# Performance work log

Hardware: AMD Instinct MI355X
Metric: run time of the kernel (lower is better)

The kernel has to match this reference:

```python
import jax, jax.numpy as jnp
import numpy as np

N_HEADS = 16

def _rel_emb(table, len_q, len_k):
    # table: [2P+1, d] -> [len_q, len_k, d] via clipped relative distance lookup
    P = (table.shape[0] - 1) // 2
    rel = jnp.arange(len_k)[None, :] - jnp.arange(len_q)[:, None]
    idx = jnp.clip(rel, -P, P) + P
    return table[idx]

def setup_inputs() -> dict:
    key = jax.random.key(0)
    ks = jax.random.split(key, 13)
    B, S, E = 2, 2048, 1024
    P = 128
    d = E // N_HEADS
    s = 0.02
    return {
        "q": jax.random.normal(ks[0], (B, S, E), jnp.float32),
        "k": jax.random.normal(ks[1], (B, S, E), jnp.float32),
        "v": jax.random.normal(ks[2], (B, S, E), jnp.float32),
        "Wq": jax.random.normal(ks[3], (E, E), jnp.float32) * s,
        "bq": jnp.zeros((E,), jnp.float32),
        "Wk": jax.random.normal(ks[4], (E, E), jnp.float32) * s,
        "bk": jnp.zeros((E,), jnp.float32),
        "Wv": jax.random.normal(ks[5], (E, E), jnp.float32) * s,
        "bv": jnp.zeros((E,), jnp.float32),
        "Wo": jax.random.normal(ks[6], (E, E), jnp.float32) * s,
        "bo": jnp.zeros((E,), jnp.float32),
        "rk_table": jax.random.normal(ks[7], (2 * P + 1, d), jnp.float32) * s,
        "rv_table": jax.random.normal(ks[8], (2 * P + 1, d), jnp.float32) * s,
    }

def reference(q, k, v, Wq, bq, Wk, bk, Wv, bv, Wo, bo, rk_table, rv_table):
    B, Sq, E = q.shape
    Sk = k.shape[1]
    H = N_HEADS
    d = E // H
    scale = jnp.sqrt(jnp.asarray(d, q.dtype))

    qh = (q @ Wq.T + bq).reshape(B, Sq, H, d).transpose(0, 2, 1, 3)  # [B,H,Sq,d]
    kh = (k @ Wk.T + bk).reshape(B, Sk, H, d).transpose(0, 2, 1, 3)
    vh = (v @ Wv.T + bv).reshape(B, Sk, H, d).transpose(0, 2, 1, 3)

    qk = jnp.einsum('bhqd,bhkd->bhqk', qh, kh)
    r_k = _rel_emb(rk_table, Sq, Sk)                 # [Sq,Sk,d]
    q_rk = jnp.einsum('bhqd,qkd->bhqk', qh, r_k)
    attn = jax.nn.softmax((qk + q_rk) / scale, axis=-1)  # dropout p=0

    w1 = jnp.einsum('bhqk,bhkd->bhqd', attn, vh)
    r_v = _rel_emb(rv_table, Sq, Sk)
    w2 = jnp.einsum('bhqk,qkd->bhqd', attn, r_v)

    out = (w1 + w2).transpose(0, 2, 1, 3).reshape(B, Sq, E)
    return out @ Wo.T + bo
```

## Files before the change

### kernel.cpp

```cpp
#include <hip/hip_runtime.h>
#include <hip/hip_bf16.h>
#include <cstdint>
#include <cstddef>

#define NH   16
#define DH   64
#define SQ   2048
#define NB   2
#define EM   1024
#define NREL 257
#define QSTR 258
#define SCL  0.18033688f

typedef unsigned short ushort_t;
using bf16x8 = __attribute__((ext_vector_type(8))) __bf16;
using bf16x4 = __attribute__((ext_vector_type(4))) __bf16;
using f32x4  = __attribute__((ext_vector_type(4))) float;
#define MFMA16(a, b, c) __builtin_amdgcn_mfma_f32_16x16x32_bf16(a, b, c, 0, 0, 0)

__device__ __forceinline__ ushort_t f2bf(float f) {
    union { __bf16 h; ushort_t u; } x; x.h = (__bf16)f; return x.u;
}
__device__ __forceinline__ float bf2f(ushort_t u) {
    union { unsigned u; float f; } x; x.u = ((unsigned)u) << 16;
    return x.f;
}
__device__ __forceinline__ uint2 pack4(float a, float b, float c, float d) {
    union { bf16x4 v; uint2 u; } x;
    x.v = (bf16x4){ (__bf16)a, (__bf16)b, (__bf16)c, (__bf16)d };
    return x.u;
}
__device__ __forceinline__ int kperm(int x) {
    return (x & ~63) | ((x & 15) << 2) | ((x >> 4) & 3);
}

__global__ __launch_bounds__(256)
void cvt3(const float* __restrict__ a, const float* __restrict__ b,
          const float* __restrict__ c, ushort_t* __restrict__ oa,
          ushort_t* __restrict__ ob, ushort_t* __restrict__ oc, int n)
{
    const float* in = blockIdx.y == 0 ? a : (blockIdx.y == 1 ? b : c);
    ushort_t* out   = blockIdx.y == 0 ? oa : (blockIdx.y == 1 ? ob : oc);
    int i = (blockIdx.x * 256 + threadIdx.x) * 8;
    if (i < n) {
        float4 v0 = *reinterpret_cast<const float4*>(in + i);
        float4 v1 = *reinterpret_cast<const float4*>(in + i + 4);
        uint2 lo = pack4(v0.x, v0.y, v0.z, v0.w);
        uint2 hi = pack4(v1.x, v1.y, v1.z, v1.w);
        *reinterpret_cast<uint4*>(out + i) = make_uint4(lo.x, lo.y, hi.x, hi.y);
    }
}
__global__ __launch_bounds__(256)
void cvt4(const float* __restrict__ a, const float* __restrict__ b,
          const float* __restrict__ c, const float* __restrict__ d,
          ushort_t* __restrict__ oa, ushort_t* __restrict__ ob,
          ushort_t* __restrict__ oc, ushort_t* __restrict__ od, int n)
{
    const float* in = blockIdx.y == 0 ? a : (blockIdx.y == 1 ? b :
                      (blockIdx.y == 2 ? c : d));
    ushort_t* out   = blockIdx.y == 0 ? oa : (blockIdx.y == 1 ? ob :
                      (blockIdx.y == 2 ? oc : od));
    int i = (blockIdx.x * 256 + threadIdx.x) * 8;
    if (i < n) {
        float4 v0 = *reinterpret_cast<const float4*>(in + i);
        float4 v1 = *reinterpret_cast<const float4*>(in + i + 4);
        uint2 lo = pack4(v0.x, v0.y, v0.z, v0.w);
        uint2 hi = pack4(v1.x, v1.y, v1.z, v1.w);
        *reinterpret_cast<uint4*>(out + i) = make_uint4(lo.x, lo.y, hi.x, hi.y);
    }
}

__global__ __launch_bounds__(256)
void prep_tables(const float* __restrict__ rv, const float* __restrict__ rk,
                 ushort_t* __restrict__ rvT, ushort_t* __restrict__ rkb)
{
    int idx = blockIdx.x * 256 + threadIdx.x;
    if (idx < 64 * 256) {
        int d = idx >> 8, c = idx & 255;
        rvT[d * 256 + kperm(c)] = f2bf(rv[(size_t)(c + 1) * DH + d]);
    }
    idx -= 64 * 256;
    if (idx >= 0 && idx < 272 * 64) {
        int j = idx >> 6, d2 = idx & 63;
        rkb[idx] = (j < NREL) ? f2bf(rk[(size_t)j * DH + d2]) : (ushort_t)0;
    }
}

template<int MODE>
__global__ __launch_bounds__(256)
void gemm_bt(const ushort_t* __restrict__ A, const ushort_t* __restrict__ W,
             const float* __restrict__ bias, void* __restrict__ dstv,
             int M, int N, int K)
{
    __shared__ ushort_t As[128 * 40];
    __shared__ ushort_t Bs[128 * 40];
    const int t = threadIdx.x, lane = t & 63;
    const int wv = t >> 6, wr = wv >> 1, wc = wv & 1;
    const int g = lane >> 4, c16 = lane & 15;

    const int nwg = gridDim.x * gridDim.y;
    int flat = blockIdx.y * gridDim.x + blockIdx.x;
    int rm = (flat & 7) * (nwg >> 3) + (flat >> 3);
    const int n0 = (rm % gridDim.x) * 128;
    const int m0 = (rm / gridDim.x) * 128;

    f32x4 acc[4][4];
#pragma unroll
    for (int i = 0; i < 4; ++i)
#pragma unroll
        for (int j = 0; j < 4; ++j) acc[i][j] = (f32x4){0.f, 0.f, 0.f, 0.f};

    for (int k0 = 0; k0 < K; k0 += 32) {
        __syncthreads();
#pragma unroll
        for (int l = 0; l < 2; ++l) {
            const int fid = t + 256 * l;
            const int row = fid >> 2, ch = fid & 3;
            uint4 av = *reinterpret_cast<const uint4*>(A + (size_t)(m0 + row) * K + k0 + ch * 8);
            uint4 wv4 = *reinterpret_cast<const uint4*>(W + (size_t)(n0 + row) * K + k0 + ch * 8);
            *reinterpret_cast<uint4*>(As + row * 40 + ch * 8) = av;
            *reinterpret_cast<uint4*>(Bs + row * 40 + ch * 8) = wv4;
        }
        __syncthreads();

        bf16x8 af[4], bfr[4];
#pragma unroll
        for (int i = 0; i < 4; ++i)
            af[i] = *reinterpret_cast<const bf16x8*>(As + (wr * 64 + i * 16 + c16) * 40 + g * 8);
#pragma unroll
        for (int j = 0; j < 4; ++j)
            bfr[j] = *reinterpret_cast<const bf16x8*>(Bs + (wc * 64 + j * 16 + c16) * 40 + g * 8);
#pragma unroll
        for (int i = 0; i < 4; ++i)
#pragma unroll
            for (int j = 0; j < 4; ++j)
                acc[i][j] = MFMA16(af[i], bfr[j], acc[i][j]);
    }

#pragma unroll
    for (int j = 0; j < 4; ++j) {
        const int n = n0 + wc * 64 + j * 16 + c16;
        const float bn = bias[n];
#pragma unroll
        for (int i = 0; i < 4; ++i) {
#pragma unroll
            for (int r = 0; r < 4; ++r) {
                const int m = m0 + wr * 64 + i * 16 + 4 * g + r;
                const float vv = acc[i][j][r] + bn;
                if (MODE == 0) {
                    ((float*)dstv)[(size_t)m * N + n] = vv;
                } else {
                    const int b = m >> 11, s = m & (SQ - 1);
                    const int h = n >> 6, dd = n & 63;
                    if (MODE == 1) {
                        ((ushort_t*)dstv)[(((size_t)b * NH + h) * SQ + s) * DH + dd] = f2bf(vv);
                    } else {
                        const int sp = kperm(s);
                        ((ushort_t*)dstv)[(((size_t)b * NH + h) * DH + dd) * SQ + sp] = f2bf(vv);
                    }
                }
            }
        }
    }
}

__global__ __launch_bounds__(256)
void qrel_mfma(const ushort_t* __restrict__ qh, const ushort_t* __restrict__ rkb,
               ushort_t* __restrict__ qrel)
{
    const int t = threadIdx.x, lane = t & 63, w = t >> 6;
    const int g = lane >> 4, c16 = lane & 15;
    const size_t r0 = (size_t)blockIdx.x * 64 + w * 16;

    bf16x8 af[2];
#pragma unroll
    for (int ks = 0; ks < 2; ++ks)
        af[ks] = *reinterpret_cast<const bf16x8*>(qh + (r0 + c16) * DH + ks * 32 + g * 8);

    f32x4 acc[17];
#pragma unroll
    for (int n = 0; n < 17; ++n) acc[n] = (f32x4){0.f, 0.f, 0.f, 0.f};
#pragma unroll
    for (int n = 0; n < 17; ++n)
#pragma unroll
        for (int ks = 0; ks < 2; ++ks) {
            bf16x8 bf = *reinterpret_cast<const bf16x8*>(
                rkb + (size_t)(16 * n + c16) * DH + ks * 32 + g * 8);
            acc[n] = MFMA16(af[ks], bf, acc[n]);
        }
#pragma unroll
    for (int n = 0; n < 17; ++n) {
        const int j = 16 * n + c16;
        if (j < NREL) {
#pragma unroll
            for (int r = 0; r < 4; ++r)
                qrel[(r0 + 4 * g + r) * QSTR + j] = f2bf(acc[n][r] * SCL);
        }
    }
}

__global__ __launch_bounds__(256, 4)
void attn_flash(const ushort_t* __restrict__ qh, const ushort_t* __restrict__ kh,
                const ushort_t* __restrict__ vt, const ushort_t* __restrict__ qrel,
                ushort_t* __restrict__ Ptile, float* __restrict__ w1g,
                float* __restrict__ lacg, float* __restrict__ b0g,
                float* __restrict__ b256g)
{
    __shared__ ushort_t Ks[64 * 72];
    __shared__ ushort_t Vs[64 * 72];
    __shared__ ushort_t PQs[64 * 72];

    const int t = threadIdx.x, lane = t & 63, w = t >> 6;
    const int g = lane >> 4, c16 = lane & 15;
    const int nwg = gridDim.x * gridDim.y;
    int flat = blockIdx.y * gridDim.x + blockIdx.x;
    int rmid = (flat & 7) * (nwg >> 3) + (flat >> 3);
    const int q0 = (rmid & 31) * 64;
    const int bh = rmid >> 5;
    const size_t Gbase = ((size_t)bh * 32 + (q0 >> 6)) * 5;

#pragma unroll
    for (int l = 0; l < 2; ++l) {
        const int fid = t + 256 * l;
        const int row = fid >> 3, ch = fid & 7;
        uint4 v = *reinterpret_cast<const uint4*>(
            qh + ((size_t)bh * SQ + q0 + row) * DH + ch * 8);
        *reinterpret_cast<uint4*>(PQs + row * 72 + ch * 8) = v;
    }
    __syncthreads();
    bf16x8 qf[2];
#pragma unroll
    for (int ks = 0; ks < 2; ++ks)
        qf[ks] = *reinterpret_cast<const bf16x8*>(PQs + (w * 16 + c16) * 72 + ks * 32 + g * 8);

    float q0add[4], q256add[4];
#pragma unroll
    for (int i = 0; i < 4; ++i) {
        const size_t r = (size_t)bh * SQ + q0 + w * 16 + 4 * g + i;
        q0add[i]   = bf2f(qrel[r * QSTR + 0]);
        q256add[i] = bf2f(qrel[r * QSTR + 256]);
    }

    f32x4 w1[4];
#pragma unroll
    for (int n = 0; n < 4; ++n) w1[n] = (f32x4){0.f, 0.f, 0.f, 0.f};
    float lac[4] = {0.f,0.f,0.f,0.f}, b0[4] = {0.f,0.f,0.f,0.f}, b256[4] = {0.f,0.f,0.f,0.f};

    const int row_l = t >> 3, ch_l = t & 7;
    const int row_h = row_l + 32;
    uint4 kr0, kr1, vr0, vr1;
    {
        kr0 = *reinterpret_cast<const uint4*>(kh + ((size_t)bh * SQ + row_l) * DH + ch_l * 8);
        kr1 = *reinterpret_cast<const uint4*>(kh + ((size_t)bh * SQ + row_h) * DH + ch_l * 8);
        vr0 = *reinterpret_cast<const uint4*>(vt + ((size_t)bh * DH + row_l) * SQ + ch_l * 8);
        vr1 = *reinterpret_cast<const uint4*>(vt + ((size_t)bh * DH + row_h) * SQ + ch_l * 8);
    }

    for (int k0 = 0; k0 < SQ; k0 += 64) {
        __syncthreads();
        *reinterpret_cast<uint4*>(Ks + row_l * 72 + ch_l * 8) = kr0;
        *reinterpret_cast<uint4*>(Ks + row_h * 72 + ch_l * 8) = kr1;
        *reinterpret_cast<uint4*>(Vs + row_l * 72 + ch_l * 8) = vr0;
        *reinterpret_cast<uint4*>(Vs + row_h * 72 + ch_l * 8) = vr1;
        __syncthreads();
        if (k0 + 64 < SQ) {
            kr0 = *reinterpret_cast<const uint4*>(kh + ((size_t)bh * SQ + k0 + 64 + row_l) * DH + ch_l * 8);
            kr1 = *reinterpret_cast<const uint4*>(kh + ((size_t)bh * SQ + k0 + 64 + row_h) * DH + ch_l * 8);
            vr0 = *reinterpret_cast<const uint4*>(vt + ((size_t)bh * DH + row_l) * SQ + k0 + 64 + ch_l * 8);
            vr1 = *reinterpret_cast<const uint4*>(vt + ((size_t)bh * DH + row_h) * SQ + k0 + 64 + ch_l * 8);
        }

        f32x4 s[4];
#pragma unroll
        for (int n = 0; n < 4; ++n) s[n] = (f32x4){0.f, 0.f, 0.f, 0.f};
        __builtin_amdgcn_s_setprio(1);
#pragma unroll
        for (int ks = 0; ks < 2; ++ks)
#pragma unroll
            for (int n = 0; n < 4; ++n) {
                bf16x8 kf = *reinterpret_cast<const bf16x8*>(
                    Ks + (16 * n + c16) * 72 + ks * 32 + g * 8);
                s[n] = MFMA16(qf[ks], kf, s[n]);
            }
        __builtin_amdgcn_s_setprio(0);

        const int rel0 = k0 - q0;
        float rsum[4] = {0.f, 0.f, 0.f, 0.f};
        if (rel0 <= -192 || rel0 >= 192) {
            const bool lo = rel0 < 0;
#pragma unroll
            for (int i = 0; i < 4; ++i) {
                const float add = lo ? q0add[i] : q256add[i];
#pragma unroll
                for (int n = 0; n < 4; ++n) {
                    const float p = exp2f(fmaf(s[n][i], SCL, add));
                    s[n][i] = p; rsum[i] += p;
                }
                if (lo) b0[i] += rsum[i]; else b256[i] += rsum[i];
                *reinterpret_cast<uint2*>(PQs + (w * 16 + 4 * g + i) * 72 + c16 * 4) =
                    pack4(s[0][i], s[1][i], s[2][i], s[3][i]);
            }
        } else if (rel0 == -128 || rel0 == 128) {
            const int tix = (rel0 >> 6) + 2;
#pragma unroll
            for (int i = 0; i < 4; ++i) {
                const int qloc = w * 16 + 4 * g + i;
                const int qg = q0 + qloc;
                const ushort_t* qrow = qrel + ((size_t)bh * SQ + qg) * QSTR;
                float z[4];
#pragma unroll
                for (int n = 0; n < 4; ++n) {
                    const int rel = (k0 + 16 * n + c16) - qg;
                    const int idx = rel < -128 ? 0 : (rel > 128 ? 256 : rel + 128);
                    const float p = exp2f(fmaf(s[n][i], SCL, bf2f(qrow[idx])));
                    s[n][i] = p; rsum[i] += p;
                    const bool inb = (rel >= -127) & (rel <= 127);
                    z[n] = inb ? p : 0.f;
                    if (rel <= -128)      b0[i] += p;
                    else if (rel >= 128)  b256[i] += p;
                }
                *reinterpret_cast<uint2*>(PQs + qloc * 72 + c16 * 4) =
                    pack4(s[0][i], s[1][i], s[2][i], s[3][i]);
                *reinterpret_cast<uint2*>(
                    Ptile + ((Gbase + tix) * 64 + qloc) * 64 + 4 * c16) =
                    pack4(z[0], z[1], z[2], z[3]);
            }
        } else {
            const int tix = (rel0 >> 6) + 2;
#pragma unroll
            for (int i = 0; i < 4; ++i) {
                const int qloc = w * 16 + 4 * g + i;
                const int qg = q0 + qloc;
                const ushort_t* qrow = qrel + ((size_t)bh * SQ + qg) * QSTR;
#pragma unroll
                for (int n = 0; n < 4; ++n) {
                    const int rel = (k0 + 16 * n + c16) - qg;
                    const float p = exp2f(fmaf(s[n][i], SCL, bf2f(qrow[rel + 128])));
                    s[n][i] = p; rsum[i] += p;
                }
                const uint2 pk = pack4(s[0][i], s[1][i], s[2][i], s[3][i]);
                *reinterpret_cast<uint2*>(PQs + qloc * 72 + c16 * 4) = pk;
                *reinterpret_cast<uint2*>(
                    Ptile + ((Gbase + tix) * 64 + qloc) * 64 + 4 * c16) = pk;
            }
        }
#pragma unroll
        for (int i = 0; i < 4; ++i) lac[i] += rsum[i];

        __builtin_amdgcn_s_setprio(1);
#pragma unroll
        for (int ks = 0; ks < 2; ++ks) {
            bf16x8 pf = *reinterpret_cast<const bf16x8*>(
                PQs + (w * 16 + c16) * 72 + ks * 32 + g * 8);
#pragma unroll
            for (int n = 0; n < 4; ++n) {
                bf16x8 vf = *reinterpret_cast<const bf16x8*>(
                    Vs + (16 * n + c16) * 72 + ks * 32 + g * 8);
                w1[n] = MFMA16(pf, vf, w1[n]);
            }
        }
        __builtin_amdgcn_s_setprio(0);
    }

#pragma unroll
    for (int m = 1; m < 16; m <<= 1)
#pragma unroll
        for (int i = 0; i < 4; ++i) {
            lac[i]  += __shfl_xor(lac[i],  m, 64);
            b0[i]   += __shfl_xor(b0[i],   m, 64);
            b256[i] += __shfl_xor(b256[i], m, 64);
        }
    if (c16 == 0) {
#pragma unroll
        for (int i = 0; i < 4; ++i) {
            const size_t row = (size_t)bh * SQ + q0 + w * 16 + 4 * g + i;
            lacg[row] = lac[i]; b0g[row] = b0[i]; b256g[row] = b256[i];
        }
    }
#pragma unroll
    for (int n = 0; n < 4; ++n)
#pragma unroll
        for (int i = 0; i < 4; ++i) {
            const size_t row = (size_t)bh * SQ + q0 + w * 16 + 4 * g + i;
            w1g[row * DH + 16 * n + c16] = w1[n][i];
        }
}

__global__ __launch_bounds__(256)
void band_gemm(const ushort_t* __restrict__ Ptile, const ushort_t* __restrict__ rvT,
               const float* __restrict__ rv_f32, const float* __restrict__ w1g,
               const float* __restrict__ lacg, const float* __restrict__ b0g,
               const float* __restrict__ b256g, ushort_t* __restrict__ wout)
{
    __shared__ ushort_t Pband[64 * 264];
    const int t = threadIdx.x, lane = t & 63, w = t >> 6;
    const int g = lane >> 4, c16 = lane & 15;
    const int G = blockIdx.x;
    const size_t r0 = (size_t)G * 64;
    const int q0 = (G & 31) * 64;

    for (int i = t; i < 64 * 264 / 2; i += 256)
        reinterpret_cast<unsigned*>(Pband)[i] = 0u;
    __syncthreads();

    for (int u = t; u < 5 * 64 * 16; u += 256) {
        const int tix = u >> 10;
        const int kt0 = q0 + (tix - 2) * 64;
        if (kt0 < 0 || kt0 >= SQ) continue;
        const int qloc = (u >> 4) & 63;
        const int c = u & 15;
        uint2 pv = *reinterpret_cast<const uint2*>(
            Ptile + (((size_t)G * 5 + tix) * 64 + qloc) * 64 + 4 * c);
        const ushort_t* pe = reinterpret_cast<const ushort_t*>(&pv);
        const int relbase = (tix - 2) * 64 - qloc + 127;
#pragma unroll
        for (int n = 0; n < 4; ++n) {
            const int x = relbase + 16 * n + c;
            if (x >= 0 && x <= 254)
                Pband[qloc * 264 + ((x & ~63) | ((x & 15) << 2) | ((x >> 4) & 3))] = pe[n];
        }
    }
    if (t < 64) Pband[t * 264 + 255] = f2bf(b256g[r0 + t]);
    __syncthreads();

    f32x4 acc[4];
#pragma unroll
    for (int n = 0; n < 4; ++n) acc[n] = (f32x4){0.f, 0.f, 0.f, 0.f};
#pragma unroll
    for (int ks = 0; ks < 8; ++ks) {
        bf16x8 pm = *reinterpret_cast<const bf16x8*>(
            Pband + (w * 16 + c16) * 264 + ks * 32 + g * 8);
#pragma unroll
        for (int n = 0; n < 4; ++n) {
            bf16x8 rf = *reinterpret_cast<const bf16x8*>(
                rvT + (size_t)(16 * n + c16) * 256 + ks * 32 + g * 8);
            acc[n] = MFMA16(pm, rf, acc[n]);
        }
    }

#pragma unroll
    for (int i = 0; i < 4; ++i) {
        const size_t row = r0 + w * 16 + 4 * g + i;
        const float inv = 1.0f / lacg[row];
        const float vb0 = b0g[row];
        const int b = (int)(row >> 15), h = (int)((row >> 11) & 15), s = (int)(row & 2047);
#pragma unroll
        for (int n = 0; n < 4; ++n) {
            const int col = 16 * n + c16;
            const float val = (w1g[row * DH + col] + acc[n][i] + vb0 * rv_f32[col]) * inv;
            wout[(((size_t)b * SQ + s) * NH + h) * DH + col] = f2bf(val);
        }
    }
}

extern "C" void kernel_launch(void* const* d_in, const int* in_sizes, int n_in,
                              void* d_out, int out_size, void* d_ws, size_t ws_size,
                              hipStream_t stream)
{
    const float* q  = (const float*)d_in[0];
    const float* k  = (const float*)d_in[1];
    const float* v  = (const float*)d_in[2];
    const float* Wq = (const float*)d_in[3];
    const float* bq = (const float*)d_in[4];
    const float* Wk = (const float*)d_in[5];
    const float* bk = (const float*)d_in[6];
    const float* Wv = (const float*)d_in[7];
    const float* bv = (const float*)d_in[8];
    const float* Wo = (const float*)d_in[9];
    const float* bo = (const float*)d_in[10];
    const float* rk = (const float*)d_in[11];
    const float* rv = (const float*)d_in[12];

    char* ws = (char*)d_ws;
    auto alloc = [&](size_t bytes) { char* p = ws; ws += bytes; return p; };
    const size_t QB = (size_t)NB * SQ * EM * 2;
    const size_t WB = (size_t)EM * EM * 2;
    const size_t NR = (size_t)NB * NH * SQ;

    char* region0 = alloc(NR * 320 * 2);
    ushort_t* Ptile = (ushort_t*)region0;
    ushort_t* qbf = (ushort_t*)region0;
    ushort_t* kbf = (ushort_t*)(region0 + QB);
    ushort_t* vbf = (ushort_t*)(region0 + 2 * QB);
    ushort_t* Wqb = (ushort_t*)(region0 + 3 * QB);
    ushort_t* Wkb = (ushort_t*)(region0 + 3 * QB + WB);
    ushort_t* Wvb = (ushort_t*)(region0 + 3 * QB + 2 * WB);

    ushort_t* Wob  = (ushort_t*)alloc(WB);
    ushort_t* qhb  = (ushort_t*)alloc(QB);
    ushort_t* khb  = (ushort_t*)alloc(QB);
    ushort_t* vtb  = (ushort_t*)alloc(QB);
    ushort_t* wbuf = (ushort_t*)alloc(QB);
    ushort_t* rvT  = (ushort_t*)alloc(64 * 256 * 2);
    ushort_t* rkb  = (ushort_t*)alloc(272 * 64 * 2);
    ushort_t* qrel = (ushort_t*)alloc(NR * QSTR * 2);
    float*    w1g  = (float*)alloc(NR * DH * 4);
    float*    lacg = (float*)alloc(NR * 4);
    float*    b0g  = (float*)alloc(NR * 4);
    float*    b256g= (float*)alloc(NR * 4);

    const int NQ = NB * SQ * EM;
    const int NW = EM * EM;
    cvt3<<<dim3(NQ / 2048, 3), 256, 0, stream>>>(q, k, v, qbf, kbf, vbf, NQ);
    cvt4<<<dim3(NW / 2048, 4), 256, 0, stream>>>(Wq, Wk, Wv, Wo, Wqb, Wkb, Wvb, Wob, NW);
    prep_tables<<<132, 256, 0, stream>>>(rv, rk, rvT, rkb);

    const int M = NB * SQ;
    dim3 gg(EM / 128, M / 128);
    gemm_bt<1><<<gg, 256, 0, stream>>>(qbf, Wqb, bq, qhb, M, EM, EM);
    gemm_bt<1><<<gg, 256, 0, stream>>>(kbf, Wkb, bk, khb, M, EM, EM);
    gemm_bt<2><<<gg, 256, 0, stream>>>(vbf, Wvb, bv, vtb, M, EM, EM);
    qrel_mfma<<<(int)(NR / 64), 256, 0, stream>>>(qhb, rkb, qrel);

    attn_flash<<<dim3(32, 32), 256, 0, stream>>>(qhb, khb, vtb, qrel,
                                                 Ptile, w1g, lacg, b0g, b256g);
    band_gemm<<<(int)(NR / 64), 256, 0, stream>>>(Ptile, rvT, rv, w1g, lacg,
                                                  b0g, b256g, wbuf);
    gemm_bt<0><<<gg, 256, 0, stream>>>(wbuf, Wob, bo, d_out, M, EM, EM);
}
```

Measured before the change: 279.8 us.

## Fuse fp32-to-bf16 conversion into GEMM loads and enlarge attention query tile

Removes the standalone conversion kernels for activations and weights, converting fp32 to bf16 inside the GEMM tile loads instead. The flash-attention kernel now processes 128 queries per block (two 64-row subtiles per wave) to reuse K/V tiles from LDS, uses XOR-swizzled LDS layouts in place of padded rows, and drops to 2 blocks per CU. The band tiles, band_gemm indexing and workspace layout are adjusted to match, with wbuf aliased onto qrel. In exchange, the GEMMs now read fp32 weights and activations from global memory every tile, and occupancy for attention is lower.

```diff
diff --git a/kernel.cpp b/kernel.cpp
--- a/kernel.cpp
+++ b/kernel.cpp
@@ -33,41 +33,8 @@
 __device__ __forceinline__ int kperm(int x) {
     return (x & ~63) | ((x & 15) << 2) | ((x >> 4) & 3);
 }
-
-__global__ __launch_bounds__(256)
-void cvt3(const float* __restrict__ a, const float* __restrict__ b,
-          const float* __restrict__ c, ushort_t* __restrict__ oa,
-          ushort_t* __restrict__ ob, ushort_t* __restrict__ oc, int n)
-{
-    const float* in = blockIdx.y == 0 ? a : (blockIdx.y == 1 ? b : c);
-    ushort_t* out   = blockIdx.y == 0 ? oa : (blockIdx.y == 1 ? ob : oc);
-    int i = (blockIdx.x * 256 + threadIdx.x) * 8;
-    if (i < n) {
-        float4 v0 = *reinterpret_cast<const float4*>(in + i);
-        float4 v1 = *reinterpret_cast<const float4*>(in + i + 4);
-        uint2 lo = pack4(v0.x, v0.y, v0.z, v0.w);
-        uint2 hi = pack4(v1.x, v1.y, v1.z, v1.w);
-        *reinterpret_cast<uint4*>(out + i) = make_uint4(lo.x, lo.y, hi.x, hi.y);
-    }
-}
-__global__ __launch_bounds__(256)
-void cvt4(const float* __restrict__ a, const float* __restrict__ b,
-          const float* __restrict__ c, const float* __restrict__ d,
-          ushort_t* __restrict__ oa, ushort_t* __restrict__ ob,
-          ushort_t* __restrict__ oc, ushort_t* __restrict__ od, int n)
-{
-    const float* in = blockIdx.y == 0 ? a : (blockIdx.y == 1 ? b :
-                      (blockIdx.y == 2 ? c : d));
-    ushort_t* out   = blockIdx.y == 0 ? oa : (blockIdx.y == 1 ? ob :
-                      (blockIdx.y == 2 ? oc : od));
-    int i = (blockIdx.x * 256 + threadIdx.x) * 8;
-    if (i < n) {
-        float4 v0 = *reinterpret_cast<const float4*>(in + i);
-        float4 v1 = *reinterpret_cast<const float4*>(in + i + 4);
-        uint2 lo = pack4(v0.x, v0.y, v0.z, v0.w);
-        uint2 hi = pack4(v1.x, v1.y, v1.z, v1.w);
-        *reinterpret_cast<uint4*>(out + i) = make_uint4(lo.x, lo.y, hi.x, hi.y);
-    }
+__device__ __forceinline__ int lswz(int row, int byteoff) {
+    return row * 128 + (byteoff ^ ((row & 7) << 4));
 }
 
 __global__ __launch_bounds__(256)
@@ -86,9 +53,9 @@
     }
 }
 
-template<int MODE>
+template<int MODE, int ACVT>
 __global__ __launch_bounds__(256)
-void gemm_bt(const ushort_t* __restrict__ A, const ushort_t* __restrict__ W,
+void gemm_bt(const void* __restrict__ Av, const float* __restrict__ Wf,
              const float* __restrict__ bias, void* __restrict__ dstv,
              int M, int N, int K)
 {
@@ -116,10 +83,23 @@
         for (int l = 0; l < 2; ++l) {
             const int fid = t + 256 * l;
             const int row = fid >> 2, ch = fid & 3;
-            uint4 av = *reinterpret_cast<const uint4*>(A + (size_t)(m0 + row) * K + k0 + ch * 8);
-            uint4 wv4 = *reinterpret_cast<const uint4*>(W + (size_t)(n0 + row) * K + k0 + ch * 8);
-            *reinterpret_cast<uint4*>(As + row * 40 + ch * 8) = av;
-            *reinterpret_cast<uint4*>(Bs + row * 40 + ch * 8) = wv4;
+            if (ACVT) {
+                const float* Af = (const float*)Av;
+                float4 a0 = *reinterpret_cast<const float4*>(Af + (size_t)(m0 + row) * K + k0 + ch * 8);
+                float4 a1 = *reinterpret_cast<const float4*>(Af + (size_t)(m0 + row) * K + k0 + ch * 8 + 4);
+                uint2 lo = pack4(a0.x, a0.y, a0.z, a0.w);
+                uint2 hi = pack4(a1.x, a1.y, a1.z, a1.w);
+                *reinterpret_cast<uint4*>(As + row * 40 + ch * 8) = make_uint4(lo.x, lo.y, hi.x, hi.y);
+            } else {
+                const ushort_t* Ab = (const ushort_t*)Av;
+                *reinterpret_cast<uint4*>(As + row * 40 + ch * 8) =
+                    *reinterpret_cast<const uint4*>(Ab + (size_t)(m0 + row) * K + k0 + ch * 8);
+            }
+            float4 w0 = *reinterpret_cast<const float4*>(Wf + (size_t)(n0 + row) * K + k0 + ch * 8);
+            float4 w1_ = *reinterpret_cast<const float4*>(Wf + (size_t)(n0 + row) * K + k0 + ch * 8 + 4);
+            uint2 lo = pack4(w0.x, w0.y, w0.z, w0.w);
+            uint2 hi = pack4(w1_.x, w1_.y, w1_.z, w1_.w);
+            *reinterpret_cast<uint4*>(Bs + row * 40 + ch * 8) = make_uint4(lo.x, lo.y, hi.x, hi.y);
         }
         __syncthreads();
 
@@ -199,69 +179,74 @@
     }
 }
 
-__global__ __launch_bounds__(256, 4)
+__global__ __launch_bounds__(256, 2)
 void attn_flash(const ushort_t* __restrict__ qh, const ushort_t* __restrict__ kh,
                 const ushort_t* __restrict__ vt, const ushort_t* __restrict__ qrel,
                 ushort_t* __restrict__ Ptile, float* __restrict__ w1g,
                 float* __restrict__ lacg, float* __restrict__ b0g,
                 float* __restrict__ b256g)
 {
-    __shared__ ushort_t Ks[64 * 72];
-    __shared__ ushort_t Vs[64 * 72];
-    __shared__ ushort_t PQs[64 * 72];
+    __shared__ ushort_t Ks[64 * 64];
+    __shared__ ushort_t Vs[64 * 64];
+    __shared__ ushort_t PQs[128 * 64];
+    char* Ksb = (char*)Ks; char* Vsb = (char*)Vs; char* PQb = (char*)PQs;
 
     const int t = threadIdx.x, lane = t & 63, w = t >> 6;
     const int g = lane >> 4, c16 = lane & 15;
-    const int nwg = gridDim.x * gridDim.y;
     int flat = blockIdx.y * gridDim.x + blockIdx.x;
-    int rmid = (flat & 7) * (nwg >> 3) + (flat >> 3);
-    const int q0 = (rmid & 31) * 64;
-    const int bh = rmid >> 5;
-    const size_t Gbase = ((size_t)bh * 32 + (q0 >> 6)) * 5;
-
-#pragma unroll
-    for (int l = 0; l < 2; ++l) {
+    int rmid = (flat & 7) * 64 + (flat >> 3);
+    const int q0 = (rmid & 15) * 128;
+    const int bh = rmid >> 4;
+    const size_t Gbase = (size_t)rmid * 6;
+
+#pragma unroll
+    for (int l = 0; l < 4; ++l) {
         const int fid = t + 256 * l;
         const int row = fid >> 3, ch = fid & 7;
         uint4 v = *reinterpret_cast<const uint4*>(
             qh + ((size_t)bh * SQ + q0 + row) * DH + ch * 8);
-        *reinterpret_cast<uint4*>(PQs + row * 72 + ch * 8) = v;
+        *reinterpret_cast<uint4*>(PQb + lswz(row, ch * 16)) = v;
     }
     __syncthreads();
-    bf16x8 qf[2];
-#pragma unroll
-    for (int ks = 0; ks < 2; ++ks)
-        qf[ks] = *reinterpret_cast<const bf16x8*>(PQs + (w * 16 + c16) * 72 + ks * 32 + g * 8);
-
-    float q0add[4], q256add[4];
-#pragma unroll
-    for (int i = 0; i < 4; ++i) {
-        const size_t r = (size_t)bh * SQ + q0 + w * 16 + 4 * g + i;
-        q0add[i]   = bf2f(qrel[r * QSTR + 0]);
-        q256add[i] = bf2f(qrel[r * QSTR + 256]);
-    }
-
-    f32x4 w1[4];
-#pragma unroll
-    for (int n = 0; n < 4; ++n) w1[n] = (f32x4){0.f, 0.f, 0.f, 0.f};
-    float lac[4] = {0.f,0.f,0.f,0.f}, b0[4] = {0.f,0.f,0.f,0.f}, b256[4] = {0.f,0.f,0.f,0.f};
+    bf16x8 qf[2][2];
+#pragma unroll
+    for (int st = 0; st < 2; ++st)
+#pragma unroll
+        for (int ks = 0; ks < 2; ++ks)
+            qf[st][ks] = *reinterpret_cast<const bf16x8*>(
+                PQb + lswz(w * 16 + st * 64 + c16, ks * 64 + g * 16));
+
+    float q0add[2][4], q256add[2][4];
+#pragma unroll
+    for (int st = 0; st < 2; ++st)
+#pragma unroll
+        for (int i = 0; i < 4; ++i) {
+            const size_t r = (size_t)bh * SQ + q0 + w * 16 + st * 64 + 4 * g + i;
+            q0add[st][i]   = bf2f(qrel[r * QSTR + 0]);
+            q256add[st][i] = bf2f(qrel[r * QSTR + 256]);
+        }
+
+    f32x4 w1[2][4];
+#pragma unroll
+    for (int st = 0; st < 2; ++st)
+#pragma unroll
+        for (int n = 0; n < 4; ++n) w1[st][n] = (f32x4){0.f, 0.f, 0.f, 0.f};
+    float lac[2][4] = {}, b0[2][4] = {}, b256[2][4] = {};
 
     const int row_l = t >> 3, ch_l = t & 7;
     const int row_h = row_l + 32;
     uint4 kr0, kr1, vr0, vr1;
-    {
-        kr0 = *reinterpret_cast<const uint4*>(kh + ((size_t)bh * SQ + row_l) * DH + ch_l * 8);
-        kr1 = *reinterpret_cast<const uint4*>(kh + ((size_t)bh * SQ + row_h) * DH + ch_l * 8);
-        vr0 = *reinterpret_cast<const uint4*>(vt + ((size_t)bh * DH + row_l) * SQ + ch_l * 8);
-        vr1 = *reinterpret_cast<const uint4*>(vt + ((size_t)bh * DH + row_h) * SQ + ch_l * 8);
-    }
+    kr0 = *reinterpret_cast<const uint4*>(kh + ((size_t)bh * SQ + row_l) * DH + ch_l * 8);
+    kr1 = *reinterpret_cast<const uint4*>(kh + ((size_t)bh * SQ + row_h) * DH + ch_l * 8);
+    vr0 = *reinterpret_cast<const uint4*>(vt + ((size_t)bh * DH + row_l) * SQ + ch_l * 8);
+    vr1 = *reinterpret_cast<const uint4*>(vt + ((size_t)bh * DH + row_h) * SQ + ch_l * 8);
 
     for (int k0 = 0; k0 < SQ; k0 += 64) {
         __syncthreads();
-        *reinterpret_cast<uint4*>(Ks + row_l * 72 + ch_l * 8) = kr0;
-        *reinterpret_cast<uint4*>(Ks + row_h * 72 + ch_l * 8) = kr1;
-        *reinterpret_cast<uint4*>(Vs + row_l * 72 + ch_l * 8) = vr0;
-        *reinterpret_cast<uint4*>(Vs + row_h * 72 + ch_l * 8) = vr1;
+        *reinterpret_cast<uint4*>(Ksb + lswz(row_l, ch_l * 16)) = kr0;
+        *reinterpret_cast<uint4*>(Ksb + lswz(row_h, ch_l * 16)) = kr1;
+        *reinterpret_cast<uint4*>(Vsb + lswz(row_l, ch_l * 16)) = vr0;
+        *reinterpret_cast<uint4*>(Vsb + lswz(row_h, ch_l * 16)) = vr1;
         __syncthreads();
         if (k0 + 64 < SQ) {
             kr0 = *reinterpret_cast<const uint4*>(kh + ((size_t)bh * SQ + k0 + 64 + row_l) * DH + ch_l * 8);
@@ -270,120 +255,141 @@
             vr1 = *reinterpret_cast<const uint4*>(vt + ((size_t)bh * DH + row_h) * SQ + k0 + 64 + ch_l * 8);
         }
 
-        f32x4 s[4];
-#pragma unroll
-        for (int n = 0; n < 4; ++n) s[n] = (f32x4){0.f, 0.f, 0.f, 0.f};
-        __builtin_amdgcn_s_setprio(1);
-#pragma unroll
-        for (int ks = 0; ks < 2; ++ks)
-#pragma unroll
-            for (int n = 0; n < 4; ++n) {
-                bf16x8 kf = *reinterpret_cast<const bf16x8*>(
-                    Ks + (16 * n + c16) * 72 + ks * 32 + g * 8);
-                s[n] = MFMA16(qf[ks], kf, s[n]);
+        f32x4 s[2][4];
+#pragma unroll
+        for (int st = 0; st < 2; ++st)
+#pragma unroll
+            for (int n = 0; n < 4; ++n) s[st][n] = (f32x4){0.f, 0.f, 0.f, 0.f};
+        {
+            bf16x8 kf[4][2];
+#pragma unroll
+            for (int n = 0; n < 4; ++n)
+#pragma unroll
+                for (int ks = 0; ks < 2; ++ks)
+                    kf[n][ks] = *reinterpret_cast<const bf16x8*>(
+                        Ksb + lswz(16 * n + c16, ks * 64 + g * 16));
+            __builtin_amdgcn_s_setprio(1);
+#pragma unroll
+            for (int st = 0; st < 2; ++st)
+#pragma unroll
+                for (int ks = 0; ks < 2; ++ks)
+#pragma unroll
+                    for (int n = 0; n < 4; ++n)
+                        s[st][n] = MFMA16(qf[st][ks], kf[n][ks], s[st][n]);
+            __builtin_amdgcn_s_setprio(0);
+        }
+
+        const int rel0 = k0 - q0;
+        if (rel0 <= -192 || rel0 >= 256) {
+            const bool lo = rel0 < 0;
+#pragma unroll
+            for (int st = 0; st < 2; ++st)
+#pragma unroll
+                for (int i = 0; i < 4; ++i) {
+                    const float add = lo ? q0add[st][i] : q256add[st][i];
+                    float rs = 0.f;
+#pragma unroll
+                    for (int n = 0; n < 4; ++n) {
+                        const float p = exp2f(fmaf(s[st][n][i], SCL, add));
+                        s[st][n][i] = p; rs += p;
+                    }
+                    lac[st][i] += rs;
+                    if (lo) b0[st][i] += rs; else b256[st][i] += rs;
+                    const int qloc = w * 16 + st * 64 + 4 * g + i;
+                    *reinterpret_cast<uint2*>(PQb + lswz(qloc, c16 * 8)) =
+                        pack4(s[st][0][i], s[st][1][i], s[st][2][i], s[st][3][i]);
+                }
+        } else {
+            const int tix = (rel0 + 128) >> 6;
+            const bool mixed = (rel0 < 0) | (rel0 > 64);
+#pragma unroll
+            for (int st = 0; st < 2; ++st)
+#pragma unroll
+                for (int i = 0; i < 4; ++i) {
+                    const int qloc = w * 16 + st * 64 + 4 * g + i;
+                    const int qg = q0 + qloc;
+                    const ushort_t* qrow = qrel + ((size_t)bh * SQ + qg) * QSTR;
+                    float z[4];
+                    float rs = 0.f;
+#pragma unroll
+                    for (int n = 0; n < 4; ++n) {
+                        const int rel = rel0 + 16 * n + c16 - qloc;
+                        int idx;
+                        if (mixed) idx = rel < -128 ? 0 : (rel > 128 ? 256 : rel + 128);
+                        else       idx = rel + 128;
+                        const float p = exp2f(fmaf(s[st][n][i], SCL, bf2f(qrow[idx])));
+                        s[st][n][i] = p; rs += p;
+                        if (mixed) {
+                            const bool inb = (rel >= -127) & (rel <= 127);
+                            z[n] = inb ? p : 0.f;
+                            if (rel <= -128)      b0[st][i] += p;
+                            else if (rel >= 128)  b256[st][i] += p;
+                        } else z[n] = p;
+                    }
+                    lac[st][i] += rs;
+                    *reinterpret_cast<uint2*>(PQb + lswz(qloc, c16 * 8)) =
+                        pack4(s[st][0][i], s[st][1][i], s[st][2][i], s[st][3][i]);
+                    *reinterpret_cast<uint2*>(
+                        Ptile + ((Gbase + tix) * 128 + qloc) * 64 + 4 * c16) =
+                        pack4(z[0], z[1], z[2], z[3]);
+                }
+        }
+
+        {
+            bf16x8 vf[4][2];
+#pragma unroll
+            for (int n = 0; n < 4; ++n)
+#pragma unroll
+                for (int ks = 0; ks < 2; ++ks)
+                    vf[n][ks] = *reinterpret_cast<const bf16x8*>(
+                        Vsb + lswz(16 * n + c16, ks * 64 + g * 16));
+            bf16x8 pf[2][2];
+#pragma unroll
+            for (int st = 0; st < 2; ++st)
+#pragma unroll
+                for (int ks = 0; ks < 2; ++ks)
+                    pf[st][ks] = *reinterpret_cast<const bf16x8*>(
+                        PQb + lswz(w * 16 + st * 64 + c16, ks * 64 + g * 16));
+            __builtin_amdgcn_s_setprio(1);
+#pragma unroll
+            for (int st = 0; st < 2; ++st)
+#pragma unroll
+                for (int ks = 0; ks < 2; ++ks)
+#pragma unroll
+                    for (int n = 0; n < 4; ++n)
+                        w1[st][n] = MFMA16(pf[st][ks], vf[n][ks], w1[st][n]);
+            __builtin_amdgcn_s_setprio(0);
+        }
+    }
+
+#pragma unroll
+    for (int m = 1; m < 16; m <<= 1)
+#pragma unroll
+        for (int st = 0; st < 2; ++st)
+#pragma unroll
+            for (int i = 0; i < 4; ++i) {
+                lac[st][i]  += __shfl_xor(lac[st][i],  m, 64);
+                b0[st][i]   += __shfl_xor(b0[st][i],   m, 64);
+                b256[st][i] += __shfl_xor(b256[st][i], m, 64);
             }
-        __builtin_amdgcn_s_setprio(0);
-
-        const int rel0 = k0 - q0;
-        float rsum[4] = {0.f, 0.f, 0.f, 0.f};
-        if (rel0 <= -192 || rel0 >= 192) {
-            const bool lo = rel0 < 0;
+    if (c16 == 0) {
+#pragma unroll
+        for (int st = 0; st < 2; ++st)
 #pragma unroll
             for (int i = 0; i < 4; ++i) {
-                const float add = lo ? q0add[i] : q256add[i];
-#pragma unroll
-                for (int n = 0; n < 4; ++n) {
-                    const float p = exp2f(fmaf(s[n][i], SCL, add));
-                    s[n][i] = p; rsum[i] += p;
-                }
-                if (lo) b0[i] += rsum[i]; else b256[i] += rsum[i];
-                *reinterpret_cast<uint2*>(PQs + (w * 16 + 4 * g + i) * 72 + c16 * 4) =
-                    pack4(s[0][i], s[1][i], s[2][i], s[3][i]);
+                const size_t row = (size_t)bh * SQ + q0 + w * 16 + st * 64 + 4 * g + i;
+                lacg[row] = lac[st][i]; b0g[row] = b0[st][i]; b256g[row] = b256[st][i];
             }
-        } else if (rel0 == -128 || rel0 == 128) {
-            const int tix = (rel0 >> 6) + 2;
+    }
+#pragma unroll
+    for (int st = 0; st < 2; ++st)
+#pragma unroll
+        for (int n = 0; n < 4; ++n)
 #pragma unroll
             for (int i = 0; i < 4; ++i) {
-                const int qloc = w * 16 + 4 * g + i;
-                const int qg = q0 + qloc;
-                const ushort_t* qrow = qrel + ((size_t)bh * SQ + qg) * QSTR;
-                float z[4];
-#pragma unroll
-                for (int n = 0; n < 4; ++n) {
-                    const int rel = (k0 + 16 * n + c16) - qg;
-                    const int idx = rel < -128 ? 0 : (rel > 128 ? 256 : rel + 128);
-                    const float p = exp2f(fmaf(s[n][i], SCL, bf2f(qrow[idx])));
-                    s[n][i] = p; rsum[i] += p;
-                    const bool inb = (rel >= -127) & (rel <= 127);
-                    z[n] = inb ? p : 0.f;
-                    if (rel <= -128)      b0[i] += p;
-                    else if (rel >= 128)  b256[i] += p;
-                }
-                *reinterpret_cast<uint2*>(PQs + qloc * 72 + c16 * 4) =
-                    pack4(s[0][i], s[1][i], s[2][i], s[3][i]);
-                *reinterpret_cast<uint2*>(
-                    Ptile + ((Gbase + tix) * 64 + qloc) * 64 + 4 * c16) =
-                    pack4(z[0], z[1], z[2], z[3]);
+                const size_t row = (size_t)bh * SQ + q0 + w * 16 + st * 64 + 4 * g + i;
+                w1g[row * DH + 16 * n + c16] = w1[st][n][i];
             }
-        } else {
-            const int tix = (rel0 >> 6) + 2;
-#pragma unroll
-            for (int i = 0; i < 4; ++i) {
-                const int qloc = w * 16 + 4 * g + i;
-                const int qg = q0 + qloc;
-                const ushort_t* qrow = qrel + ((size_t)bh * SQ + qg) * QSTR;
-#pragma unroll
-                for (int n = 0; n < 4; ++n) {
-                    const int rel = (k0 + 16 * n + c16) - qg;
-                    const float p = exp2f(fmaf(s[n][i], SCL, bf2f(qrow[rel + 128])));
-                    s[n][i] = p; rsum[i] += p;
-                }
-                const uint2 pk = pack4(s[0][i], s[1][i], s[2][i], s[3][i]);
-                *reinterpret_cast<uint2*>(PQs + qloc * 72 + c16 * 4) = pk;
-                *reinterpret_cast<uint2*>(
-                    Ptile + ((Gbase + tix) * 64 + qloc) * 64 + 4 * c16) = pk;
-            }
-        }
-#pragma unroll
-        for (int i = 0; i < 4; ++i) lac[i] += rsum[i];
-
-        __builtin_amdgcn_s_setprio(1);
-#pragma unroll
-        for (int ks = 0; ks < 2; ++ks) {
-            bf16x8 pf = *reinterpret_cast<const bf16x8*>(
-                PQs + (w * 16 + c16) * 72 + ks * 32 + g * 8);
-#pragma unroll
-            for (int n = 0; n < 4; ++n) {
-                bf16x8 vf = *reinterpret_cast<const bf16x8*>(
-                    Vs + (16 * n + c16) * 72 + ks * 32 + g * 8);
-                w1[n] = MFMA16(pf, vf, w1[n]);
-            }
-        }
-        __builtin_amdgcn_s_setprio(0);
-    }
-
-#pragma unroll
-    for (int m = 1; m < 16; m <<= 1)
-#pragma unroll
-        for (int i = 0; i < 4; ++i) {
-            lac[i]  += __shfl_xor(lac[i],  m, 64);
-            b0[i]   += __shfl_xor(b0[i],   m, 64);
-            b256[i] += __shfl_xor(b256[i], m, 64);
-        }
-    if (c16 == 0) {
-#pragma unroll
-        for (int i = 0; i < 4; ++i) {
-            const size_t row = (size_t)bh * SQ + q0 + w * 16 + 4 * g + i;
-            lacg[row] = lac[i]; b0g[row] = b0[i]; b256g[row] = b256[i];
-        }
-    }
-#pragma unroll
-    for (int n = 0; n < 4; ++n)
-#pragma unroll
-        for (int i = 0; i < 4; ++i) {
-            const size_t row = (size_t)bh * SQ + q0 + w * 16 + 4 * g + i;
-            w1g[row * DH + 16 * n + c16] = w1[n][i];
-        }
 }
 
 __global__ __launch_bounds__(256)
@@ -395,29 +401,32 @@
     __shared__ ushort_t Pband[64 * 264];
     const int t = threadIdx.x, lane = t & 63, w = t >> 6;
     const int g = lane >> 4, c16 = lane & 15;
-    const int G = blockIdx.x;
-    const size_t r0 = (size_t)G * 64;
-    const int q0 = (G & 31) * 64;
+    const int blk = blockIdx.x;
+    const size_t r0 = (size_t)blk * 64;
+    const int G = blk >> 1;
+    const int half = blk & 1;
+    const int q0 = (G & 15) * 128;
 
     for (int i = t; i < 64 * 264 / 2; i += 256)
         reinterpret_cast<unsigned*>(Pband)[i] = 0u;
     __syncthreads();
 
-    for (int u = t; u < 5 * 64 * 16; u += 256) {
+    for (int u = t; u < 6 * 64 * 16; u += 256) {
         const int tix = u >> 10;
-        const int kt0 = q0 + (tix - 2) * 64;
+        const int kt0 = q0 + tix * 64 - 128;
         if (kt0 < 0 || kt0 >= SQ) continue;
-        const int qloc = (u >> 4) & 63;
+        const int qloc64 = (u >> 4) & 63;
         const int c = u & 15;
+        const int qloc128 = half * 64 + qloc64;
         uint2 pv = *reinterpret_cast<const uint2*>(
-            Ptile + (((size_t)G * 5 + tix) * 64 + qloc) * 64 + 4 * c);
+            Ptile + (((size_t)G * 6 + tix) * 128 + qloc128) * 64 + 4 * c);
         const ushort_t* pe = reinterpret_cast<const ushort_t*>(&pv);
-        const int relbase = (tix - 2) * 64 - qloc + 127;
+        const int relbase = tix * 64 - 1 - qloc128;
 #pragma unroll
         for (int n = 0; n < 4; ++n) {
             const int x = relbase + 16 * n + c;
             if (x >= 0 && x <= 254)
-                Pband[qloc * 264 + ((x & ~63) | ((x & 15) << 2) | ((x >> 4) & 3))] = pe[n];
+                Pband[qloc64 * 264 + ((x & ~63) | ((x & 15) << 2) | ((x >> 4) & 3))] = pe[n];
         }
     }
     if (t < 64) Pband[t * 264 + 255] = f2bf(b256g[r0 + t]);
@@ -474,47 +483,34 @@
     char* ws = (char*)d_ws;
     auto alloc = [&](size_t bytes) { char* p = ws; ws += bytes; return p; };
     const size_t QB = (size_t)NB * SQ * EM * 2;
-    const size_t WB = (size_t)EM * EM * 2;
     const size_t NR = (size_t)NB * NH * SQ;
 
-    char* region0 = alloc(NR * 320 * 2);
-    ushort_t* Ptile = (ushort_t*)region0;
-    ushort_t* qbf = (ushort_t*)region0;
-    ushort_t* kbf = (ushort_t*)(region0 + QB);
-    ushort_t* vbf = (ushort_t*)(region0 + 2 * QB);
-    ushort_t* Wqb = (ushort_t*)(region0 + 3 * QB);
-    ushort_t* Wkb = (ushort_t*)(region0 + 3 * QB + WB);
-    ushort_t* Wvb = (ushort_t*)(region0 + 3 * QB + 2 * WB);
-
-    ushort_t* Wob  = (ushort_t*)alloc(WB);
+    ushort_t* Ptile = (ushort_t*)alloc((size_t)512 * 6 * 128 * 64 * 2);
     ushort_t* qhb  = (ushort_t*)alloc(QB);
     ushort_t* khb  = (ushort_t*)alloc(QB);
     ushort_t* vtb  = (ushort_t*)alloc(QB);
-    ushort_t* wbuf = (ushort_t*)alloc(QB);
     ushort_t* rvT  = (ushort_t*)alloc(64 * 256 * 2);
     ushort_t* rkb  = (ushort_t*)alloc(272 * 64 * 2);
-    ushort_t* qrel = (ushort_t*)alloc(NR * QSTR * 2);
+    char*     qrel_region = alloc(NR * QSTR * 2);
+    ushort_t* qrel = (ushort_t*)qrel_region;
+    ushort_t* wbuf = (ushort_t*)qrel_region;
     float*    w1g  = (float*)alloc(NR * DH * 4);
     float*    lacg = (float*)alloc(NR * 4);
     float*    b0g  = (float*)alloc(NR * 4);
     float*    b256g= (float*)alloc(NR * 4);
 
-    const int NQ = NB * SQ * EM;
-    const int NW = EM * EM;
-    cvt3<<<dim3(NQ / 2048, 3), 256, 0, stream>>>(q, k, v, qbf, kbf, vbf, NQ);
-    cvt4<<<dim3(NW / 2048, 4), 256, 0, stream>>>(Wq, Wk, Wv, Wo, Wqb, Wkb, Wvb, Wob, NW);
     prep_tables<<<132, 256, 0, stream>>>(rv, rk, rvT, rkb);
 
     const int M = NB * SQ;
     dim3 gg(EM / 128, M / 128);
-    gemm_bt<1><<<gg, 256, 0, stream>>>(qbf, Wqb, bq, qhb, M, EM, EM);
-    gemm_bt<1><<<gg, 256, 0, stream>>>(kbf, Wkb, bk, khb, M, EM, EM);
-    gemm_bt<2><<<gg, 256, 0, stream>>>(vbf, Wvb, bv, vtb, M, EM, EM);
+    gemm_bt<1, 1><<<gg, 256, 0, stream>>>(q, Wq, bq, qhb, M, EM, EM);
+    gemm_bt<1, 1><<<gg, 256, 0, stream>>>(k, Wk, bk, khb, M, EM, EM);
+    gemm_bt<2, 1><<<gg, 256, 0, stream>>>(v, Wv, bv, vtb, M, EM, EM);
     qrel_mfma<<<(int)(NR / 64), 256, 0, stream>>>(qhb, rkb, qrel);
 
-    attn_flash<<<dim3(32, 32), 256, 0, stream>>>(qhb, khb, vtb, qrel,
+    attn_flash<<<dim3(16, 32), 256, 0, stream>>>(qhb, khb, vtb, qrel,
                                                  Ptile, w1g, lacg, b0g, b256g);
     band_gemm<<<(int)(NR / 64), 256, 0, stream>>>(Ptile, rvT, rv, w1g, lacg,
                                                   b0g, b256g, wbuf);
-    gemm_bt<0><<<gg, 256, 0, stream>>>(wbuf, Wob, bo, d_out, M, EM, EM);
-}
+    gemm_bt<0, 0><<<gg, 256, 0, stream>>>(wbuf, Wo, bo, d_out, M, EM, EM);
+}
```

After: 330.1 us. +18.0%, slower.
